# Performance work log

Hardware: AMD Instinct MI355X
Metric: run time of the kernel (lower is better)

The kernel has to match this reference:

```python
import jax, jax.numpy as jnp
import numpy as np

H = W = 20
NVARS = 4          # n_predictor_vars
NK = 12            # n_conv2d_kernels
NF = NK + NVARS + 1  # 17 augmented channels (conv + original + time)
SIGLEN = NF + NF * NF  # 306, depth-2 signature length
T_END = 1.0        # self.T in the module


def setup_inputs() -> dict:
    key = jax.random.key(0)
    ks = jax.random.split(key, 8)
    B, T = 64, 96
    x = jax.random.normal(ks[0], (B, T, NVARS, H, W), dtype=jnp.float32)
    conv_w = jax.random.normal(ks[1], (NK, NVARS, 3, 3), dtype=jnp.float32) * 0.1
    conv_b = jax.random.normal(ks[2], (NK,), dtype=jnp.float32) * 0.01
    d_in = SIGLEN * H * W  # 122400

    def lin(k, fan_in, fan_out):
        return jax.random.normal(k, (fan_in, fan_out), dtype=jnp.float32) / np.float32(np.sqrt(fan_in))

    w1, b1 = lin(ks[3], d_in, 32), jnp.zeros((32,), jnp.float32)
    w2, b2 = lin(ks[4], 32, 32), jnp.zeros((32,), jnp.float32)
    w3, b3 = lin(ks[5], 32, 32), jnp.zeros((32,), jnp.float32)
    w4, b4 = lin(ks[6], 32, 1), jnp.zeros((1,), jnp.float32)
    return {"x": x, "conv_w": conv_w, "conv_b": conv_b,
            "w1": w1, "b1": b1, "w2": w2, "b2": b2,
            "w3": w3, "b3": b3, "w4": w4, "b4": b4}


def reference(x, conv_w, conv_b, w1, b1, w2, b2, w3, b3, w4, b4):
    B, T = x.shape[0], x.shape[1]
    # Batched conv over all timesteps at once (the torch code loops over t).
    xi = x.reshape(B * T, NVARS, H, W)
    y = jax.lax.conv_general_dilated(
        xi, conv_w, window_strides=(1, 1), padding='SAME',
        dimension_numbers=('NCHW', 'OIHW', 'NCHW'))
    y = y + conv_b[None, :, None, None]
    y = y.reshape(B, T, NK, H, W)
    # Dropout3d is identity in eval mode.
    # Augment: [conv features, original values, time channel] along channel dim.
    tch = jnp.linspace(0.0, T_END, T, dtype=x.dtype).reshape(1, T, 1, 1, 1)
    tch = jnp.broadcast_to(tch, (B, T, 1, H, W))
    feat = jnp.concatenate([y, x, tch], axis=2)        # (B, T, NF, H, W)
    path = jnp.transpose(feat, (0, 3, 4, 1, 2))        # (B, H, W, T, NF)
    # Depth-2 path signature (Chen closed form):
    # level1 = sum dx; level2 = sum_{i<j} dx_i (x) dx_j + 0.5 sum_i dx_i (x) dx_i
    dx = path[..., 1:, :] - path[..., :-1, :]          # (B,H,W,T-1,NF)
    csum = jnp.cumsum(dx, axis=-2)                     # inclusive prefix sums
    lvl1 = csum[..., -1, :]                            # (B,H,W,NF)
    # (exclusive prefix) + 0.5*dx = csum - 0.5*dx -> single contracted einsum
    lvl2 = jnp.einsum('bhwti,bhwtj->bhwij', csum - 0.5 * dx, dx)
    sig = jnp.concatenate([lvl1, lvl2.reshape(B, H, W, NF * NF)], axis=-1)  # (B,H,W,306)
    flat = sig.reshape(B, H * W * SIGLEN)
    h = jax.nn.relu(flat @ w1 + b1)
    h = jax.nn.relu(h @ w2 + b2)
    h = jax.nn.relu(h @ w3 + b3)
    return h @ w4 + b4                                 # (B, 1)
```

## Files before the change

kernel.cpp:

```cpp
#include <hip/hip_runtime.h>

#define HH 20
#define WW 20
#define TT 96
#define BB 64
#define SIG 306
#define NFC 17
#define TSTRIDE 260
#define CHUNK 16
#define NCHUNK 6
#define XT 199
#define KTOT 122400
#define KSLAB 120
#define NSLAB 2
#define NKBLK 510
#define LDT 66

typedef float float4u __attribute__((ext_vector_type(4), aligned(4)));

__global__ __launch_bounds__(256) void sig_kernel(
    const float* __restrict__ x,
    const float* __restrict__ cw,
    float* __restrict__ sig)
{
  __shared__ __align__(16) float feat[15 * TSTRIDE + 256 + 8];
  __shared__ __align__(16) float xs[CHUNK * XT];

  const int tid = threadIdx.x;
  const int blk = blockIdx.x;
  const int b = blk / 25;
  const int tile = blk % 25;
  const int th4 = (tile / 5) * 4, tw4 = (tile % 5) * 4;
  const float* xb0 = x + (size_t)b * TT * 1600;

  int g_off[9], l_off[9];
  #pragma unroll
  for (int r = 0; r < 9; r++) {
    int idx = r * 256 + tid;
    int t = idx / 144, q = idx % 144;
    int ci = q / 36, pos = q % 36, row = pos / 6, col = pos % 6;
    int gr = th4 - 1 + row, gc = tw4 - 1 + col;
    bool valid = (gr >= 0 && gr < HH && gc >= 0 && gc < WW);
    g_off[r] = valid ? (t * 1600 + ci * 400 + gr * WW + gc) : -1;
    l_off[r] = t * XT + ci * 48 + row * 8 + col;
  }

  const int cpix = tid >> 4, ctt = tid & 15;
  const int cpy = cpix >> 2, cpx = cpix & 3;

  const int p2 = tid >> 4;
  const int rr = tid & 15, it = rr >> 2, jt = rr & 3;
  const int i0 = it * 4, j0 = jt * 4;

  float accv[4][4];
  float f0a[4], f0b[4], pa[4], pb[4], fsum[4];
  float rg[9];
  #pragma unroll
  for (int i = 0; i < 4; i++) {
    #pragma unroll
    for (int j = 0; j < 4; j++) accv[i][j] = 0.f;
  }

  auto loadrg = [&](int chunk) {
    const float* xbc = xb0 + (size_t)chunk * CHUNK * 1600;
    #pragma unroll
    for (int r = 0; r < 9; r++)
      rg[r] = (g_off[r] >= 0) ? xbc[g_off[r]] : 0.f;
  };
  auto writexs = [&]() {
    #pragma unroll
    for (int r = 0; r < 9; r++) xs[l_off[r]] = rg[r];
  };

  auto conv = [&]() {
    float win[4][9];
    const int wb2 = ctt * XT;
    #pragma unroll
    for (int ci = 0; ci < 4; ci++)
      #pragma unroll
      for (int dy = 0; dy < 3; dy++)
        #pragma unroll
        for (int dxx = 0; dxx < 3; dxx++)
          win[ci][dy * 3 + dxx] = xs[wb2 + ci * 48 + (cpy + dy) * 8 + (cpx + dxx)];

    float fk[12];
    #pragma unroll
    for (int k = 0; k < 12; k++) {
      float a = 0.f;
      #pragma unroll
      for (int ci = 0; ci < 4; ci++) {
        #pragma unroll
        for (int p = 0; p < 9; p++)
          a += win[ci][p] * cw[k * 36 + ci * 9 + p];
      }
      fk[k] = a;
    }
    float* fr = &feat[ctt * TSTRIDE + cpix * 16];
    *reinterpret_cast<float4*>(fr + 0)  = make_float4(fk[0], fk[1], fk[2], fk[3]);
    *reinterpret_cast<float4*>(fr + 4)  = make_float4(fk[4], fk[5], fk[6], fk[7]);
    *reinterpret_cast<float4*>(fr + 8)  = make_float4(fk[8], fk[9], fk[10], fk[11]);
    *reinterpret_cast<float4*>(fr + 12) = make_float4(win[0][4], win[1][4], win[2][4], win[3][4]);
  };

  auto p2step = [&](int tt) {
    const float* row = &feat[tt * TSTRIDE + p2 * 16];
    const float4 a4 = *reinterpret_cast<const float4*>(row + i0);
    const float4 b4 = *reinterpret_cast<const float4*>(row + j0);
    float fa[4] = {a4.x, a4.y, a4.z, a4.w};
    float fb[4] = {b4.x, b4.y, b4.z, b4.w};
    float sa[4], db[4];
    #pragma unroll
    for (int i = 0; i < 4; i++) { sa[i] = fa[i] + pa[i]; db[i] = fb[i] - pb[i]; }
    #pragma unroll
    for (int i = 0; i < 4; i++)
      #pragma unroll
      for (int j = 0; j < 4; j++) accv[i][j] += sa[i] * db[j];
    #pragma unroll
    for (int i = 0; i < 4; i++) { fsum[i] += fa[i]; pa[i] = fa[i]; pb[i] = fb[i]; }
  };

  loadrg(0);
  writexs();
  __syncthreads();
  conv();
  loadrg(1);
  __syncthreads();
  {
    const float* r0 = &feat[p2 * 16];
    const float4 a4 = *reinterpret_cast<const float4*>(r0 + i0);
    const float4 b4 = *reinterpret_cast<const float4*>(r0 + j0);
    f0a[0] = a4.x; f0a[1] = a4.y; f0a[2] = a4.z; f0a[3] = a4.w;
    f0b[0] = b4.x; f0b[1] = b4.y; f0b[2] = b4.z; f0b[3] = b4.w;
    #pragma unroll
    for (int i = 0; i < 4; i++) { pa[i] = f0a[i]; pb[i] = f0b[i]; fsum[i] = f0a[i]; }
  }
  #pragma unroll
  for (int tt = 1; tt < CHUNK; tt++) p2step(tt);

  for (int chunk = 1; chunk < NCHUNK; chunk++) {
    writexs();
    __syncthreads();
    conv();
    if (chunk < NCHUNK - 1) loadrg(chunk + 1);
    __syncthreads();
    #pragma unroll
    for (int tt = 0; tt < CHUNK; tt++) p2step(tt);
  }

  {
    const int ph = th4 + (p2 >> 2), pw = tw4 + (p2 & 3);
    float* sb = sig + (size_t)b * KTOT + (size_t)(ph * WW + pw) * SIG;
    float lv1b[4];
    #pragma unroll
    for (int j = 0; j < 4; j++) lv1b[j] = pb[j] - f0b[j];
    #pragma unroll
    for (int ii = 0; ii < 4; ii++) {
      float4u v;
      #pragma unroll
      for (int jj = 0; jj < 4; jj++)
        v[jj] = 0.5f * accv[ii][jj] - f0a[ii] * lv1b[jj];
      *reinterpret_cast<float4u*>(sb + NFC + (i0 + ii) * NFC + j0) = v;
    }
    if (jt == 0) {
      #pragma unroll
      for (int ii = 0; ii < 4; ii++) {
        const int c = i0 + ii;
        const float f0 = f0a[ii], f95 = pa[ii], fs = fsum[ii];
        sb[c] = f95 - f0;
        sb[NFC + c * NFC + 16] = (fs - 95.5f * f0 - 0.5f * f95) * (1.f / 95.f);
        sb[NFC + 16 * NFC + c] = (95.5f * f95 + 0.5f * f0 - fs) * (1.f / 95.f);
      }
      if (it == 0) { sb[16] = 1.0f; sb[NFC + 16 * NFC + 16] = 0.5f; }
    }
  }
}

template<bool ATOMIC>
__global__ __launch_bounds__(256) void mlp1_gemm(
    const float* __restrict__ sig, const float* __restrict__ w1,
    float* __restrict__ part)
{
  __shared__ __align__(16) float ldsT[KSLAB * LDT];
  __shared__ __align__(16) float wls[KSLAB * 32];
  const int tid = threadIdx.x;
  const int n = tid & 31, bq = tid >> 5;
  const int k0 = blockIdx.x * (KSLAB * NSLAB);

  float a8[8];
  #pragma unroll
  for (int i = 0; i < 8; i++) a8[i] = 0.f;

  float rA[30], rW[15];
  auto loadslab = [&](int s) {
    const int ks = k0 + s * KSLAB;
    #pragma unroll
    for (int r = 0; r < 30; r++) {
      int idx = r * 256 + tid;
      int b = idx / KSLAB, kk = idx % KSLAB;
      rA[r] = sig[(size_t)b * KTOT + ks + kk];
    }
    #pragma unroll
    for (int r = 0; r < 15; r++)
      rW[r] = w1[(size_t)ks * 32 + r * 256 + tid];
  };

  loadslab(0);
  for (int s = 0; s < NSLAB; s++) {
    if (s) __syncthreads();
    #pragma unroll
    for (int r = 0; r < 30; r++) {
      int idx = r * 256 + tid;
      int b = idx / KSLAB, kk = idx % KSLAB;
      ldsT[kk * LDT + b] = rA[r];
    }
    #pragma unroll
    for (int r = 0; r < 15; r++)
      wls[r * 256 + tid] = rW[r];
    __syncthreads();
    if (s + 1 < NSLAB) loadslab(s + 1);

    #pragma unroll 4
    for (int kk = 0; kk < KSLAB; kk++) {
      const float w = wls[kk * 32 + n];
      const float4 s0 = *reinterpret_cast<const float4*>(&ldsT[kk * LDT + bq * 8]);
      const float4 s1 = *reinterpret_cast<const float4*>(&ldsT[kk * LDT + bq * 8 + 4]);
      a8[0] += s0.x * w; a8[1] += s0.y * w; a8[2] += s0.z * w; a8[3] += s0.w * w;
      a8[4] += s1.x * w; a8[5] += s1.y * w; a8[6] += s1.z * w; a8[7] += s1.w * w;
    }
  }

  if (ATOMIC) {
    #pragma unroll
    for (int i = 0; i < 8; i++)
      atomicAdd(&part[(bq * 8 + i) * 32 + n], a8[i]);
  } else {
    const size_t pb = (size_t)blockIdx.x * (BB * 32);
    #pragma unroll
    for (int i = 0; i < 8; i++)
      part[pb + (bq * 8 + i) * 32 + n] = a8[i];
  }
}

__global__ __launch_bounds__(256) void mlp_tail(
    const float* __restrict__ part, int npart, const float* __restrict__ b1,
    const float* __restrict__ w2, const float* __restrict__ b2,
    const float* __restrict__ w3, const float* __restrict__ b3,
    const float* __restrict__ w4, const float* __restrict__ b4,
    float* __restrict__ out)
{
  __shared__ float red[8][33];
  const int tid = threadIdx.x;
  const int n = tid & 31;
  const int s = tid >> 5;
  const int b = blockIdx.x;

  float sum = 0.f;
  #pragma unroll 8
  for (int p = s; p < npart; p += 8)
    sum += part[(size_t)p * (BB * 32) + b * 32 + n];
  red[s][n] = sum;
  __syncthreads();

  if (tid < 32) {
    float acc = red[0][n];
    #pragma unroll
    for (int q = 1; q < 8; q++) acc += red[q][n];

    float h = fmaxf(acc + b1[n], 0.f);

    float v = b2[n];
    #pragma unroll
    for (int k = 0; k < 32; k++)
      v += __shfl(h, k, 64) * w2[k * 32 + n];
    h = fmaxf(v, 0.f);

    v = b3[n];
    #pragma unroll
    for (int k = 0; k < 32; k++)
      v += __shfl(h, k, 64) * w3[k * 32 + n];
    h = fmaxf(v, 0.f);

    float p = h * w4[n];
    #pragma unroll
    for (int o = 16; o >= 1; o >>= 1) p += __shfl_xor(p, o, 64);
    if (n == 0) out[b] = p + b4[0];
  }
}

extern "C" void kernel_launch(void* const* d_in, const int* in_sizes, int n_in,
                              void* d_out, int out_size, void* d_ws, size_t ws_size,
                              hipStream_t stream) {
  const float* x  = (const float*)d_in[0];
  const float* cw = (const float*)d_in[1];
  const float* w1 = (const float*)d_in[3];
  const float* b1 = (const float*)d_in[4];
  const float* w2 = (const float*)d_in[5];
  const float* b2 = (const float*)d_in[6];
  const float* w3 = (const float*)d_in[7];
  const float* b3 = (const float*)d_in[8];
  const float* w4 = (const float*)d_in[9];
  const float* b4 = (const float*)d_in[10];
  float* out = (float*)d_out;

  const size_t sig_bytes  = (size_t)BB * KTOT * sizeof(float);
  const size_t part_bytes = (size_t)NKBLK * BB * 32 * sizeof(float);
  float* sigm = (float*)d_ws;

  sig_kernel<<<dim3(1600), dim3(256), 0, stream>>>(x, cw, sigm);

  if (ws_size >= sig_bytes + part_bytes) {
    float* part = (float*)((char*)d_ws + sig_bytes);
    mlp1_gemm<false><<<dim3(NKBLK), dim3(256), 0, stream>>>(sigm, w1, part);
    mlp_tail<<<dim3(64), dim3(256), 0, stream>>>(part, NKBLK, b1, w2, b2, w3, b3, w4, b4, out);
  } else {
    float* acc = (float*)((char*)d_ws + sig_bytes);
    hipMemsetAsync(acc, 0, BB * 32 * sizeof(float), stream);
    mlp1_gemm<true><<<dim3(NKBLK), dim3(256), 0, stream>>>(sigm, w1, acc);
    mlp_tail<<<dim3(64), dim3(256), 0, stream>>>(acc, 1, b1, w2, b2, w3, b3, w4, b4, out);
  }
}
```

Before: 224.0 us.

## Fuse MLP tail into GEMM via last-block ticket, remap sig blocks, prefetch earlier

The first-layer GEMM and the MLP tail are merged into one kernel. Each block writes its partials, takes a ticket from an atomic counter, and the last 64 blocks spin until every block is done, then each reduces one batch row and runs the small MLP. This removes a kernel launch at the cost of a memset and a spin-wait. Separately, the signature kernel's block index is permuted so consecutive blocks hit different batches, and the next chunk's global load is issued before the barrier instead of after conv, to overlap it with more work.

Measured after the change: 289.9 us. +29.4%, slower.

```diff
diff --git a/kernel.cpp b/kernel.cpp
--- a/kernel.cpp
+++ b/kernel.cpp
@@ -27,7 +27,7 @@
   __shared__ __align__(16) float xs[CHUNK * XT];
 
   const int tid = threadIdx.x;
-  const int blk = blockIdx.x;
+  const int blk = (blockIdx.x & 7) * 200 + (blockIdx.x >> 3);
   const int b = blk / 25;
   const int tile = blk % 25;
   const int th4 = (tile / 5) * 4, tw4 = (tile % 5) * 4;
@@ -121,9 +121,9 @@
 
   loadrg(0);
   writexs();
+  loadrg(1);
   __syncthreads();
   conv();
-  loadrg(1);
   __syncthreads();
   {
     const float* r0 = &feat[p2 * 16];
@@ -139,9 +139,9 @@
 
   for (int chunk = 1; chunk < NCHUNK; chunk++) {
     writexs();
+    if (chunk < NCHUNK - 1) loadrg(chunk + 1);
     __syncthreads();
     conv();
-    if (chunk < NCHUNK - 1) loadrg(chunk + 1);
     __syncthreads();
     #pragma unroll
     for (int tt = 0; tt < CHUNK; tt++) p2step(tt);
@@ -175,8 +175,121 @@
   }
 }
 
-template<bool ATOMIC>
-__global__ __launch_bounds__(256) void mlp1_gemm(
+__global__ __launch_bounds__(256) void mlp1_fused(
+    const float* __restrict__ sig, const float* __restrict__ w1,
+    float* __restrict__ part, unsigned* __restrict__ counter,
+    const float* __restrict__ b1,
+    const float* __restrict__ w2, const float* __restrict__ b2,
+    const float* __restrict__ w3, const float* __restrict__ b3,
+    const float* __restrict__ w4, const float* __restrict__ b4,
+    float* __restrict__ out)
+{
+  __shared__ __align__(16) float ldsT[KSLAB * LDT];
+  __shared__ __align__(16) float wls[KSLAB * 32];
+  __shared__ unsigned ticket_s;
+  const int tid = threadIdx.x;
+  const int n = tid & 31, bq = tid >> 5;
+  const int k0 = blockIdx.x * (KSLAB * NSLAB);
+
+  float a8[8];
+  #pragma unroll
+  for (int i = 0; i < 8; i++) a8[i] = 0.f;
+
+  float rA[30], rW[15];
+  auto loadslab = [&](int s) {
+    const int ks = k0 + s * KSLAB;
+    #pragma unroll
+    for (int r = 0; r < 30; r++) {
+      int idx = r * 256 + tid;
+      int b = idx / KSLAB, kk = idx % KSLAB;
+      rA[r] = sig[(size_t)b * KTOT + ks + kk];
+    }
+    #pragma unroll
+    for (int r = 0; r < 15; r++)
+      rW[r] = w1[(size_t)ks * 32 + r * 256 + tid];
+  };
+
+  loadslab(0);
+  for (int s = 0; s < NSLAB; s++) {
+    if (s) __syncthreads();
+    #pragma unroll
+    for (int r = 0; r < 30; r++) {
+      int idx = r * 256 + tid;
+      int b = idx / KSLAB, kk = idx % KSLAB;
+      ldsT[kk * LDT + b] = rA[r];
+    }
+    #pragma unroll
+    for (int r = 0; r < 15; r++)
+      wls[r * 256 + tid] = rW[r];
+    __syncthreads();
+    if (s + 1 < NSLAB) loadslab(s + 1);
+
+    #pragma unroll 4
+    for (int kk = 0; kk < KSLAB; kk++) {
+      const float w = wls[kk * 32 + n];
+      const float4 s0 = *reinterpret_cast<const float4*>(&ldsT[kk * LDT + bq * 8]);
+      const float4 s1 = *reinterpret_cast<const float4*>(&ldsT[kk * LDT + bq * 8 + 4]);
+      a8[0] += s0.x * w; a8[1] += s0.y * w; a8[2] += s0.z * w; a8[3] += s0.w * w;
+      a8[4] += s1.x * w; a8[5] += s1.y * w; a8[6] += s1.z * w; a8[7] += s1.w * w;
+    }
+  }
+
+  {
+    const size_t pb = (size_t)blockIdx.x * (BB * 32);
+    #pragma unroll
+    for (int i = 0; i < 8; i++)
+      part[pb + (bq * 8 + i) * 32 + n] = a8[i];
+  }
+
+  __threadfence();
+  if (tid == 0) ticket_s = atomicAdd(counter, 1u);
+  __syncthreads();
+  const unsigned t = ticket_s;
+  if (t < NKBLK - 64) return;
+  const int b = NKBLK - 1 - (int)t;
+
+  if (tid == 0) {
+    while (atomicAdd(counter, 0u) < (unsigned)NKBLK)
+      __builtin_amdgcn_s_sleep(2);
+  }
+  __syncthreads();
+
+  __shared__ float red[8][33];
+  const int s8 = tid >> 5;
+  float sum = 0.f;
+  #pragma unroll 8
+  for (int p = s8; p < NKBLK; p += 8)
+    sum += part[(size_t)p * (BB * 32) + b * 32 + n];
+  red[s8][n] = sum;
+  __syncthreads();
+
+  if (tid < 32) {
+    float acc = red[0][n];
+    #pragma unroll
+    for (int q = 1; q < 8; q++) acc += red[q][n];
+
+    float h = fmaxf(acc + b1[n], 0.f);
+
+    float v = b2[n];
+    #pragma unroll
+    for (int k = 0; k < 32; k++)
+      v += __shfl(h, k, 64) * w2[k * 32 + n];
+    h = fmaxf(v, 0.f);
+
+    v = b3[n];
+    #pragma unroll
+    for (int k = 0; k < 32; k++)
+      v += __shfl(h, k, 64) * w3[k * 32 + n];
+    h = fmaxf(v, 0.f);
+
+    float p = h * w4[n];
+    #pragma unroll
+    for (int o = 16; o >= 1; o >>= 1) p += __shfl_xor(p, o, 64);
+    if (n == 0) out[b] = p + b4[0];
+  }
+}
+
+__global__ __launch_bounds__(256) void mlp1_gemm_atomic(
     const float* __restrict__ sig, const float* __restrict__ w1,
     float* __restrict__ part)
 {
@@ -190,34 +303,19 @@
   #pragma unroll
   for (int i = 0; i < 8; i++) a8[i] = 0.f;
 
-  float rA[30], rW[15];
-  auto loadslab = [&](int s) {
+  for (int s = 0; s < NSLAB; s++) {
     const int ks = k0 + s * KSLAB;
+    __syncthreads();
     #pragma unroll
     for (int r = 0; r < 30; r++) {
       int idx = r * 256 + tid;
       int b = idx / KSLAB, kk = idx % KSLAB;
-      rA[r] = sig[(size_t)b * KTOT + ks + kk];
+      ldsT[kk * LDT + b] = sig[(size_t)b * KTOT + ks + kk];
     }
     #pragma unroll
     for (int r = 0; r < 15; r++)
-      rW[r] = w1[(size_t)ks * 32 + r * 256 + tid];
-  };
-
-  loadslab(0);
-  for (int s = 0; s < NSLAB; s++) {
-    if (s) __syncthreads();
-    #pragma unroll
-    for (int r = 0; r < 30; r++) {
-      int idx = r * 256 + tid;
-      int b = idx / KSLAB, kk = idx % KSLAB;
-      ldsT[kk * LDT + b] = rA[r];
-    }
-    #pragma unroll
-    for (int r = 0; r < 15; r++)
-      wls[r * 256 + tid] = rW[r];
+      wls[r * 256 + tid] = w1[(size_t)ks * 32 + r * 256 + tid];
     __syncthreads();
-    if (s + 1 < NSLAB) loadslab(s + 1);
 
     #pragma unroll 4
     for (int kk = 0; kk < KSLAB; kk++) {
@@ -228,17 +326,9 @@
       a8[4] += s1.x * w; a8[5] += s1.y * w; a8[6] += s1.z * w; a8[7] += s1.w * w;
     }
   }
-
-  if (ATOMIC) {
-    #pragma unroll
-    for (int i = 0; i < 8; i++)
-      atomicAdd(&part[(bq * 8 + i) * 32 + n], a8[i]);
-  } else {
-    const size_t pb = (size_t)blockIdx.x * (BB * 32);
-    #pragma unroll
-    for (int i = 0; i < 8; i++)
-      part[pb + (bq * 8 + i) * 32 + n] = a8[i];
-  }
+  #pragma unroll
+  for (int i = 0; i < 8; i++)
+    atomicAdd(&part[(bq * 8 + i) * 32 + n], a8[i]);
 }
 
 __global__ __launch_bounds__(256) void mlp_tail(
@@ -265,21 +355,17 @@
     float acc = red[0][n];
     #pragma unroll
     for (int q = 1; q < 8; q++) acc += red[q][n];
-
     float h = fmaxf(acc + b1[n], 0.f);
-
     float v = b2[n];
     #pragma unroll
     for (int k = 0; k < 32; k++)
       v += __shfl(h, k, 64) * w2[k * 32 + n];
     h = fmaxf(v, 0.f);
-
     v = b3[n];
     #pragma unroll
     for (int k = 0; k < 32; k++)
       v += __shfl(h, k, 64) * w3[k * 32 + n];
     h = fmaxf(v, 0.f);
-
     float p = h * w4[n];
     #pragma unroll
     for (int o = 16; o >= 1; o >>= 1) p += __shfl_xor(p, o, 64);
@@ -308,14 +394,16 @@
 
   sig_kernel<<<dim3(1600), dim3(256), 0, stream>>>(x, cw, sigm);
 
-  if (ws_size >= sig_bytes + part_bytes) {
+  if (ws_size >= sig_bytes + part_bytes + 64) {
     float* part = (float*)((char*)d_ws + sig_bytes);
-    mlp1_gemm<false><<<dim3(NKBLK), dim3(256), 0, stream>>>(sigm, w1, part);
-    mlp_tail<<<dim3(64), dim3(256), 0, stream>>>(part, NKBLK, b1, w2, b2, w3, b3, w4, b4, out);
+    unsigned* counter = (unsigned*)((char*)d_ws + sig_bytes + part_bytes);
+    hipMemsetAsync(counter, 0, sizeof(unsigned), stream);
+    mlp1_fused<<<dim3(NKBLK), dim3(256), 0, stream>>>(
+        sigm, w1, part, counter, b1, w2, b2, w3, b3, w4, b4, out);
   } else {
     float* acc = (float*)((char*)d_ws + sig_bytes);
     hipMemsetAsync(acc, 0, BB * 32 * sizeof(float), stream);
-    mlp1_gemm<true><<<dim3(NKBLK), dim3(256), 0, stream>>>(sigm, w1, acc);
+    mlp1_gemm_atomic<<<dim3(NKBLK), dim3(256), 0, stream>>>(sigm, w1, acc);
     mlp_tail<<<dim3(64), dim3(256), 0, stream>>>(acc, 1, b1, w2, b2, w3, b3, w4, b4, out);
   }
 }
```
